# Optimization experiments

Hardware: AMD Instinct MI355X
Metric: run time of the kernel (lower is better)

Reference implementation:

```python
import jax, jax.numpy as jnp
import numpy as np

B, T, I, H, C = 512, 256, 128, 64, 3  # batch, seq_len, input_size, hidden_size, num_classes


def _lstm_dir(x, w_ih, w_hh, b, reverse):
    """Single-direction LSTM over x: (B, T, D_in) -> (B, T, H).

    Gate order matches PyTorch: i, f, g, o. b = b_ih + b_hh (combined).
    Input-to-gate GEMM is hoisted out of the scan for efficiency.
    """
    xg = jnp.einsum('bti,gi->btg', x, w_ih) + b  # (B, T, 4H)
    if reverse:
        xg = xg[:, ::-1]
    xg_t = jnp.swapaxes(xg, 0, 1)  # (T, B, 4H)
    h0 = jnp.zeros((x.shape[0], w_hh.shape[1]), x.dtype)
    c0 = jnp.zeros_like(h0)

    def step(carry, g):
        h, c = carry
        g = g + h @ w_hh.T
        i, f, gg, o = jnp.split(g, 4, axis=-1)
        i = jax.nn.sigmoid(i)
        f = jax.nn.sigmoid(f)
        gg = jnp.tanh(gg)
        o = jax.nn.sigmoid(o)
        c = f * c + i * gg
        h = o * jnp.tanh(c)
        return (h, c), h

    _, hs = jax.lax.scan(step, (h0, c0), xg_t)  # (T, B, H)
    hs = jnp.swapaxes(hs, 0, 1)  # (B, T, H)
    if reverse:
        hs = hs[:, ::-1]
    return hs


def setup_inputs() -> dict:
    key = jax.random.key(0)
    ks = jax.random.split(key, 20)
    s = 1.0 / np.sqrt(H)  # PyTorch LSTM init scale
    d = {"x": jax.random.normal(ks[0], (B, T, I), dtype=jnp.float32)}
    i = 1
    for l, d_in in [(0, I), (1, 2 * H)]:
        for suf in ["f", "r"]:
            d[f"w_ih_l{l}{suf}"] = jax.random.uniform(ks[i], (4 * H, d_in), minval=-s, maxval=s); i += 1
            d[f"w_hh_l{l}{suf}"] = jax.random.uniform(ks[i], (4 * H, H), minval=-s, maxval=s); i += 1
            d[f"b_l{l}{suf}"] = jax.random.uniform(ks[i], (4 * H,), minval=-s, maxval=s); i += 1
    d["fc_w"] = jax.random.uniform(ks[i], (C, 2 * H), minval=-s, maxval=s); i += 1
    d["fc_b"] = jax.random.uniform(ks[i], (C,), minval=-s, maxval=s)
    return d


def reference(x, w_ih_l0f, w_hh_l0f, b_l0f, w_ih_l0r, w_hh_l0r, b_l0r,
              w_ih_l1f, w_hh_l1f, b_l1f, w_ih_l1r, w_hh_l1r, b_l1r,
              fc_w, fc_b):
    # Layer 0 (bidirectional)
    h0f = _lstm_dir(x, w_ih_l0f, w_hh_l0f, b_l0f, False)
    h0r = _lstm_dir(x, w_ih_l0r, w_hh_l0r, b_l0r, True)
    x1 = jnp.concatenate([h0f, h0r], axis=-1)  # (B, T, 2H)
    # (inter-layer dropout is identity in eval mode)
    # Layer 1 (bidirectional)
    h1f = _lstm_dir(x1, w_ih_l1f, w_hh_l1f, b_l1f, False)
    h1r = _lstm_dir(x1, w_ih_l1r, w_hh_l1r, b_l1r, True)
    out = jnp.concatenate([h1f, h1r], axis=-1)  # (B, T, 2H)
    last = out[:, -1, :]  # (B, 2H); dropout is identity in eval mode
    return last @ fc_w.T + fc_b  # (B, C) logits
```

## Files before the change

### kernel.cpp

```cpp
#include <hip/hip_runtime.h>

#define TT 256
#define BB 512
#define NG 256
#define KIN 128

typedef _Float16 half2v __attribute__((ext_vector_type(2)));
typedef _Float16 half4v __attribute__((ext_vector_type(4)));
typedef _Float16 half8v __attribute__((ext_vector_type(8)));
typedef float float4v __attribute__((ext_vector_type(4)));

__device__ __forceinline__ float sig_(float x){ return 1.f/(1.f+__expf(-x)); }
__device__ __forceinline__ float th_(float x){ return fmaf(2.f, 1.f/(1.f+__expf(-2.f*x)), -1.f); }

#if __has_builtin(__builtin_amdgcn_fdot2)
__device__ __forceinline__ float fdot2_(half2v a, half2v b, float c){
  return __builtin_amdgcn_fdot2(a, b, c, false);
}
#else
__device__ __forceinline__ float fdot2_(half2v a, half2v b, float c){
  return c + (float)a[0]*(float)b[0] + (float)a[1]*(float)b[1];
}
#endif

#define SV2(v,k) __builtin_shufflevector((v),(v), 2*(k), 2*(k)+1)

__device__ __forceinline__ half4v ld4h(const float* p){
  float4v v = *reinterpret_cast<const float4v*>(p);
  half4v h; h[0]=(_Float16)v[0]; h[1]=(_Float16)v[1]; h[2]=(_Float16)v[2]; h[3]=(_Float16)v[3];
  return h;
}

__global__ __launch_bounds__(256)
void conv_weights(const float* __restrict__ s0, const float* __restrict__ s1,
                  const float* __restrict__ s2, const float* __restrict__ s3,
                  const float* __restrict__ s4, const float* __restrict__ s5,
                  _Float16* __restrict__ dst)
{
  const int bid = blockIdx.x, tid = threadIdx.x;
  const float* src; int off, idx;
  if (bid < 128)      { src=s0; off=0;      idx=bid*256+tid; }
  else if (bid < 256) { src=s1; off=32768;  idx=(bid-128)*256+tid; }
  else if (bid < 384) { src=s2; off=65536;  idx=(bid-256)*256+tid; }
  else if (bid < 448) { src=s3; off=98304;  idx=(bid-384)*256+tid; }
  else if (bid < 512) { src=s4; off=114688; idx=(bid-448)*256+tid; }
  else                { src=s5; off=131072; idx=(bid-512)*256+tid; }
  dst[off+idx] = (_Float16)src[idx];
}

template<typename AT>
__global__ __launch_bounds__(256)
void gemm_xg(const AT* __restrict__ A, const _Float16* __restrict__ W16,
             const float* __restrict__ bias, _Float16* __restrict__ Cout)
{
  __shared__ __align__(16) _Float16 aL[64][72];
  __shared__ __align__(16) _Float16 wL[256][72];
  const int tid  = threadIdx.x;
  const int wave = tid >> 6;
  const int lane = tid & 63;
  const int lr   = lane & 15;
  const int kg   = lane >> 4;
  const size_t m0 = (size_t)blockIdx.x * 64;

  float4v acc[4][4];
  #pragma unroll
  for (int a=0;a<4;a++)
    #pragma unroll
    for (int b=0;b<4;b++)
      acc[a][b] = float4v{0.f,0.f,0.f,0.f};

  for (int kc = 0; kc < KIN; kc += 64) {
    if constexpr (__is_same(AT, float)) {
      #pragma unroll
      for (int q=0;q<4;q++){
        int fi = tid + q*256;
        int r = fi >> 4, c4 = (fi & 15)*4;
        *reinterpret_cast<half4v*>(&aL[r][c4]) = ld4h(&A[(m0+(size_t)r)*KIN + kc + c4]);
      }
    } else {
      #pragma unroll
      for (int q=0;q<2;q++){
        int fi = tid + q*256;
        int r = fi >> 3, c8 = (fi & 7)*8;
        *reinterpret_cast<half8v*>(&aL[r][c8]) =
            *reinterpret_cast<const half8v*>(&A[(m0+(size_t)r)*KIN + kc + c8]);
      }
    }
    #pragma unroll
    for (int q=0;q<8;q++){
      int fi = tid + q*256;
      int n = fi >> 3, c8 = (fi & 7)*8;
      *reinterpret_cast<half8v*>(&wL[n][c8]) =
          *reinterpret_cast<const half8v*>(&W16[(size_t)n*KIN + kc + c8]);
    }
    __syncthreads();
    #pragma unroll
    for (int ks=0; ks<64; ks+=32){
      half8v af[4], bf[4];
      #pragma unroll
      for (int rt=0;rt<4;rt++)
        af[rt] = *reinterpret_cast<const half8v*>(&aL[rt*16+lr][ks + kg*8]);
      #pragma unroll
      for (int ct=0;ct<4;ct++)
        bf[ct] = *reinterpret_cast<const half8v*>(&wL[wave*64 + ct*16 + lr][ks + kg*8]);
      #pragma unroll
      for (int rt=0;rt<4;rt++)
        #pragma unroll
        for (int ct=0;ct<4;ct++)
          acc[rt][ct] = __builtin_amdgcn_mfma_f32_16x16x32_f16(af[rt], bf[ct], acc[rt][ct], 0,0,0);
    }
    __syncthreads();
  }
  #pragma unroll
  for (int ct=0;ct<4;ct++){
    const int col = wave*64 + ct*16 + lr;
    const float bv = bias[col];
    #pragma unroll
    for (int rt=0;rt<4;rt++){
      const size_t rbase = m0 + rt*16 + kg*4;
      #pragma unroll
      for (int i=0;i<4;i++)
        Cout[(rbase+(size_t)i)*NG + col] = (_Float16)(acc[rt][ct][i] + bv);
    }
  }
}

template<int MODE>
__global__ __launch_bounds__(64, 1)
void lstm_scan_w1(const _Float16* __restrict__ xgPool,
                  const _Float16* __restrict__ whhPool,
                  int nF,
                  _Float16* __restrict__ x1out, float* __restrict__ hfin)
{
  const int j = threadIdx.x;
  const bool rev = (int)blockIdx.x >= nF;
  const int b = rev ? ((int)blockIdx.x - nF) : (int)blockIdx.x;
  const size_t xgOff  = rev ? (size_t)BB*TT*NG : 0;
  const size_t whhOff = rev ? (size_t)16384 : 0;
  const _Float16* xg  = xgPool  + xgOff;
  const _Float16* whh = whhPool + whhOff;

  __shared__ __align__(16) _Float16 hs[64];

  half8v wi8[8], wf8[8], wg8[8], wo8[8];
  #pragma unroll
  for (int q=0;q<8;q++){
    wi8[q] = *reinterpret_cast<const half8v*>(&whh[(size_t)(      j)*64 + q*8]);
    wf8[q] = *reinterpret_cast<const half8v*>(&whh[(size_t)( 64 + j)*64 + q*8]);
    wg8[q] = *reinterpret_cast<const half8v*>(&whh[(size_t)(128 + j)*64 + q*8]);
    wo8[q] = *reinterpret_cast<const half8v*>(&whh[(size_t)(192 + j)*64 + q*8]);
  }
  hs[j] = (_Float16)0.f;
  float c = 0.f, h_last = 0.f;
  __syncthreads();

  const _Float16* xgb = xg + (size_t)b*TT*NG + j;
  _Float16 ring[4][4];
  #pragma unroll
  for (int u=0;u<4;u++){
    const size_t o = (size_t)(rev ? (TT-1-u) : u) * NG;
    #pragma unroll
    for (int g=0;g<4;g++) ring[u][g] = xgb[o + g*64];
  }

  for (int tb=0; tb<TT; tb+=4){
    #pragma unroll
    for (int u=0;u<4;u++){
      const int tt = tb + u;
      const int t  = rev ? (TT-1-tt) : tt;

      const float x0  = (float)ring[u][0];
      const float x1v = (float)ring[u][1];
      const float x2  = (float)ring[u][2];
      const float x3  = (float)ring[u][3];

      const int tf = tt + 4;
      if (tf < TT){
        const size_t o = (size_t)(rev ? (TT-1-tf) : tf) * NG;
        #pragma unroll
        for (int g=0;g<4;g++) ring[u][g] = xgb[o + g*64];
      }

      float ai=0.f, a2i=0.f, af=0.f, a2f=0.f, ag=0.f, a2g=0.f, ao=0.f, a2o=0.f;
      #pragma unroll
      for (int q=0;q<8;q++){
        const half8v h8 = *reinterpret_cast<const half8v*>(&hs[q*8]);
        const half2v hA = SV2(h8,0), hB = SV2(h8,1), hC = SV2(h8,2), hD = SV2(h8,3);
        ai  = fdot2_(SV2(wi8[q],0), hA, ai);  a2i = fdot2_(SV2(wi8[q],1), hB, a2i);
        ai  = fdot2_(SV2(wi8[q],2), hC, ai);  a2i = fdot2_(SV2(wi8[q],3), hD, a2i);
        af  = fdot2_(SV2(wf8[q],0), hA, af);  a2f = fdot2_(SV2(wf8[q],1), hB, a2f);
        af  = fdot2_(SV2(wf8[q],2), hC, af);  a2f = fdot2_(SV2(wf8[q],3), hD, a2f);
        ag  = fdot2_(SV2(wg8[q],0), hA, ag);  a2g = fdot2_(SV2(wg8[q],1), hB, a2g);
        ag  = fdot2_(SV2(wg8[q],2), hC, ag);  a2g = fdot2_(SV2(wg8[q],3), hD, a2g);
        ao  = fdot2_(SV2(wo8[q],0), hA, ao);  a2o = fdot2_(SV2(wo8[q],1), hB, a2o);
        ao  = fdot2_(SV2(wo8[q],2), hC, ao);  a2o = fdot2_(SV2(wo8[q],3), hD, a2o);
      }
      const float iv = sig_(x0  + (ai + a2i));
      const float fv = sig_(x1v + (af + a2f));
      const float gv = th_ (x2  + (ag + a2g));
      const float ov = sig_(x3  + (ao + a2o));

      c = fv*c + iv*gv;
      const float h = ov * th_(c);
      h_last = h;
      hs[j] = (_Float16)h;
      if constexpr (MODE==0)
        x1out[((size_t)b*TT + t)*128 + (rev ? 64 : 0) + j] = (_Float16)h;
    }
  }
  if constexpr (MODE==1)
    hfin[(size_t)b*64 + j] = h_last;
}

__global__ __launch_bounds__(256)
void final_fuse(const _Float16* __restrict__ x1, const float* __restrict__ w_ih,
                const float* __restrict__ bvec, const float* __restrict__ hfin,
                const float* __restrict__ fcw, const float* __restrict__ fcb,
                float* __restrict__ out)
{
  const int b = blockIdx.x, tid = threadIdx.x;
  __shared__ float xs[128];
  __shared__ float act[256];
  __shared__ float hall[128];
  if (tid < 128) xs[tid] = (float)x1[((size_t)b*TT + (TT-1))*128 + tid];
  __syncthreads();
  float a = bvec[tid];
  #pragma unroll
  for (int kk=0;kk<32;kk++){
    float4v wv = *reinterpret_cast<const float4v*>(&w_ih[(size_t)tid*128 + kk*4]);
    a += wv[0]*xs[kk*4] + wv[1]*xs[kk*4+1] + wv[2]*xs[kk*4+2] + wv[3]*xs[kk*4+3];
  }
  const int grp = tid>>6;
  act[tid] = (grp==2) ? th_(a) : sig_(a);
  __syncthreads();
  if (tid < 64) {
    float c = act[tid]*act[128+tid];
    float h = act[192+tid]*th_(c);
    hall[64+tid] = h;
    hall[tid] = hfin[(size_t)b*64 + tid];
  }
  __syncthreads();
  if (tid < 3) {
    float acc2 = fcb[tid];
    for (int k=0;k<128;k++) acc2 += fcw[(size_t)tid*128 + k]*hall[k];
    out[(size_t)b*3 + tid] = acc2;
  }
}

extern "C" void kernel_launch(void* const* d_in, const int* in_sizes, int n_in,
                              void* d_out, int out_size, void* d_ws, size_t ws_size,
                              hipStream_t stream) {
  const float* x        = (const float*)d_in[0];
  const float* w_ih_l0f = (const float*)d_in[1];
  const float* w_hh_l0f = (const float*)d_in[2];
  const float* b_l0f    = (const float*)d_in[3];
  const float* w_ih_l0r = (const float*)d_in[4];
  const float* w_hh_l0r = (const float*)d_in[5];
  const float* b_l0r    = (const float*)d_in[6];
  const float* w_ih_l1f = (const float*)d_in[7];
  const float* w_hh_l1f = (const float*)d_in[8];
  const float* b_l1f    = (const float*)d_in[9];
  const float* w_ih_l1r = (const float*)d_in[10];
  const float* b_l1r    = (const float*)d_in[12];
  const float* fc_w     = (const float*)d_in[13];
  const float* fc_b     = (const float*)d_in[14];
  float* out = (float*)d_out;

  const size_t XG_BYTES = (size_t)BB*TT*NG*2;
  const size_t X1_BYTES = (size_t)BB*TT*128*2;
  const size_t HF_BYTES = (size_t)BB*64*4;
  const size_t W16_BYTES = (size_t)147456*2;
  if (ws_size < 2*XG_BYTES + X1_BYTES + HF_BYTES + W16_BYTES) return;
  _Float16* xgF  = (_Float16*)d_ws;
  _Float16* xgR  = (_Float16*)((char*)d_ws + XG_BYTES);
  _Float16* x1   = (_Float16*)((char*)d_ws + 2*XG_BYTES);
  float*    hfin = (float*)   ((char*)d_ws + 2*XG_BYTES + X1_BYTES);
  _Float16* w16  = (_Float16*)((char*)d_ws + 2*XG_BYTES + X1_BYTES + HF_BYTES);
  _Float16* wih_l0f16 = w16;
  _Float16* wih_l0r16 = w16 + 32768;
  _Float16* wih_l1f16 = w16 + 65536;
  _Float16* whh_l0f16 = w16 + 98304;
  _Float16* whh_l1f16 = w16 + 131072;

  const int MBLK = (BB*TT)/64;

  conv_weights<<<576, 256, 0, stream>>>(w_ih_l0f, w_ih_l0r, w_ih_l1f,
                                        w_hh_l0f, w_hh_l0r, w_hh_l1f, w16);
  gemm_xg<float><<<MBLK, 256, 0, stream>>>(x, wih_l0f16, b_l0f, xgF);
  gemm_xg<float><<<MBLK, 256, 0, stream>>>(x, wih_l0r16, b_l0r, xgR);
  lstm_scan_w1<0><<<1024, 64, 0, stream>>>(xgF, whh_l0f16, 512, x1, nullptr);
  gemm_xg<_Float16><<<MBLK, 256, 0, stream>>>(x1, wih_l1f16, b_l1f, xgF);
  lstm_scan_w1<1><<<512, 64, 0, stream>>>(xgF, whh_l1f16, 512, nullptr, hfin);
  final_fuse<<<BB, 256, 0, stream>>>(x1, w_ih_l1r, b_l1r, hfin, fc_w, fc_b, out);
}
```

Measured before the change: 477.3 us.

## Split LSTM scan gates across four waves with LDS exchange per timestep

The recurrent scan now uses four waves per sequence instead of one. Each wave computes the h·W_hh dot product and activation for a single gate, writes it to a double-buffered LDS array, and after a block barrier every wave redundantly updates c and h. This cuts the serial dot-product work per thread per step by four and raises the number of resident waves per CU. The cost is a __syncthreads on every timestep, redundant cell-state math in all four waves, and a deeper xg prefetch ring.

```diff
diff --git a/kernel.cpp b/kernel.cpp
--- a/kernel.cpp
+++ b/kernel.cpp
@@ -126,90 +126,77 @@
 }
 
 template<int MODE>
-__global__ __launch_bounds__(64, 1)
-void lstm_scan_w1(const _Float16* __restrict__ xgPool,
+__global__ __launch_bounds__(256, 4)
+void lstm_scan_g4(const _Float16* __restrict__ xgPool,
                   const _Float16* __restrict__ whhPool,
                   int nF,
                   _Float16* __restrict__ x1out, float* __restrict__ hfin)
 {
-  const int j = threadIdx.x;
+  const int tid = threadIdx.x;
+  const int w   = tid >> 6;
+  const int j   = tid & 63;
   const bool rev = (int)blockIdx.x >= nF;
   const int b = rev ? ((int)blockIdx.x - nF) : (int)blockIdx.x;
-  const size_t xgOff  = rev ? (size_t)BB*TT*NG : 0;
-  const size_t whhOff = rev ? (size_t)16384 : 0;
-  const _Float16* xg  = xgPool  + xgOff;
-  const _Float16* whh = whhPool + whhOff;
-
-  __shared__ __align__(16) _Float16 hs[64];
-
-  half8v wi8[8], wf8[8], wg8[8], wo8[8];
-  #pragma unroll
-  for (int q=0;q<8;q++){
-    wi8[q] = *reinterpret_cast<const half8v*>(&whh[(size_t)(      j)*64 + q*8]);
-    wf8[q] = *reinterpret_cast<const half8v*>(&whh[(size_t)( 64 + j)*64 + q*8]);
-    wg8[q] = *reinterpret_cast<const half8v*>(&whh[(size_t)(128 + j)*64 + q*8]);
-    wo8[q] = *reinterpret_cast<const half8v*>(&whh[(size_t)(192 + j)*64 + q*8]);
-  }
-  hs[j] = (_Float16)0.f;
+  const _Float16* xg  = xgPool  + (rev ? (size_t)BB*TT*NG : 0);
+  const _Float16* whh = whhPool + (rev ? (size_t)16384 : 0);
+
+  __shared__ __align__(16) float acts[2][256];
+  __shared__ __align__(16) _Float16 hs4[4][64];
+
+  half8v wreg[8];
+  #pragma unroll
+  for (int q=0;q<8;q++)
+    wreg[q] = *reinterpret_cast<const half8v*>(&whh[(size_t)(w*64 + j)*64 + q*8]);
+
+  hs4[w][j] = (_Float16)0.f;
   float c = 0.f, h_last = 0.f;
-  __syncthreads();
-
-  const _Float16* xgb = xg + (size_t)b*TT*NG + j;
-  _Float16 ring[4][4];
-  #pragma unroll
-  for (int u=0;u<4;u++){
-    const size_t o = (size_t)(rev ? (TT-1-u) : u) * NG;
-    #pragma unroll
-    for (int g=0;g<4;g++) ring[u][g] = xgb[o + g*64];
-  }
-
-  for (int tb=0; tb<TT; tb+=4){
-    #pragma unroll
-    for (int u=0;u<4;u++){
+
+  const _Float16* xgb = xg + (size_t)b*TT*NG + w*64 + j;
+  _Float16 ring[8];
+  #pragma unroll
+  for (int u=0;u<8;u++)
+    ring[u] = xgb[(size_t)(rev ? (TT-1-u) : u) * NG];
+
+  for (int tb=0; tb<TT; tb+=8){
+    #pragma unroll
+    for (int u=0;u<8;u++){
       const int tt = tb + u;
       const int t  = rev ? (TT-1-tt) : tt;
 
-      const float x0  = (float)ring[u][0];
-      const float x1v = (float)ring[u][1];
-      const float x2  = (float)ring[u][2];
-      const float x3  = (float)ring[u][3];
-
-      const int tf = tt + 4;
-      if (tf < TT){
-        const size_t o = (size_t)(rev ? (TT-1-tf) : tf) * NG;
-        #pragma unroll
-        for (int g=0;g<4;g++) ring[u][g] = xgb[o + g*64];
+      const float xp = (float)ring[u];
+      const int tf = tt + 8;
+      if (tf < TT)
+        ring[u] = xgb[(size_t)(rev ? (TT-1-tf) : tf) * NG];
+
+      float a=0.f, a2=0.f;
+      #pragma unroll
+      for (int q=0;q<8;q++){
+        const half8v h8 = *reinterpret_cast<const half8v*>(&hs4[w][q*8]);
+        a  = fdot2_(SV2(wreg[q],0), SV2(h8,0), a);
+        a2 = fdot2_(SV2(wreg[q],1), SV2(h8,1), a2);
+        a  = fdot2_(SV2(wreg[q],2), SV2(h8,2), a);
+        a2 = fdot2_(SV2(wreg[q],3), SV2(h8,3), a2);
       }
-
-      float ai=0.f, a2i=0.f, af=0.f, a2f=0.f, ag=0.f, a2g=0.f, ao=0.f, a2o=0.f;
-      #pragma unroll
-      for (int q=0;q<8;q++){
-        const half8v h8 = *reinterpret_cast<const half8v*>(&hs[q*8]);
-        const half2v hA = SV2(h8,0), hB = SV2(h8,1), hC = SV2(h8,2), hD = SV2(h8,3);
-        ai  = fdot2_(SV2(wi8[q],0), hA, ai);  a2i = fdot2_(SV2(wi8[q],1), hB, a2i);
-        ai  = fdot2_(SV2(wi8[q],2), hC, ai);  a2i = fdot2_(SV2(wi8[q],3), hD, a2i);
-        af  = fdot2_(SV2(wf8[q],0), hA, af);  a2f = fdot2_(SV2(wf8[q],1), hB, a2f);
-        af  = fdot2_(SV2(wf8[q],2), hC, af);  a2f = fdot2_(SV2(wf8[q],3), hD, a2f);
-        ag  = fdot2_(SV2(wg8[q],0), hA, ag);  a2g = fdot2_(SV2(wg8[q],1), hB, a2g);
-        ag  = fdot2_(SV2(wg8[q],2), hC, ag);  a2g = fdot2_(SV2(wg8[q],3), hD, a2g);
-        ao  = fdot2_(SV2(wo8[q],0), hA, ao);  a2o = fdot2_(SV2(wo8[q],1), hB, a2o);
-        ao  = fdot2_(SV2(wo8[q],2), hC, ao);  a2o = fdot2_(SV2(wo8[q],3), hD, a2o);
-      }
-      const float iv = sig_(x0  + (ai + a2i));
-      const float fv = sig_(x1v + (af + a2f));
-      const float gv = th_ (x2  + (ag + a2g));
-      const float ov = sig_(x3  + (ao + a2o));
-
+      const float pre = xp + (a + a2);
+      acts[tt&1][w*64 + j] = (w==2) ? th_(pre) : sig_(pre);
+      __syncthreads();
+
+      const float iv = acts[tt&1][j];
+      const float fv = acts[tt&1][64+j];
+      const float gv = acts[tt&1][128+j];
+      const float ov = acts[tt&1][192+j];
       c = fv*c + iv*gv;
       const float h = ov * th_(c);
       h_last = h;
-      hs[j] = (_Float16)h;
+      hs4[w][j] = (_Float16)h;
       if constexpr (MODE==0)
-        x1out[((size_t)b*TT + t)*128 + (rev ? 64 : 0) + j] = (_Float16)h;
+        if (w == 0)
+          x1out[((size_t)b*TT + t)*128 + (rev ? 64 : 0) + j] = (_Float16)h;
     }
   }
   if constexpr (MODE==1)
-    hfin[(size_t)b*64 + j] = h_last;
+    if (w == 0)
+      hfin[(size_t)b*64 + j] = h_last;
 }
 
 __global__ __launch_bounds__(256)
@@ -288,8 +275,8 @@
                                         w_hh_l0f, w_hh_l0r, w_hh_l1f, w16);
   gemm_xg<float><<<MBLK, 256, 0, stream>>>(x, wih_l0f16, b_l0f, xgF);
   gemm_xg<float><<<MBLK, 256, 0, stream>>>(x, wih_l0r16, b_l0r, xgR);
-  lstm_scan_w1<0><<<1024, 64, 0, stream>>>(xgF, whh_l0f16, 512, x1, nullptr);
+  lstm_scan_g4<0><<<1024, 256, 0, stream>>>(xgF, whh_l0f16, 512, x1, nullptr);
   gemm_xg<_Float16><<<MBLK, 256, 0, stream>>>(x1, wih_l1f16, b_l1f, xgF);
-  lstm_scan_w1<1><<<512, 64, 0, stream>>>(xgF, whh_l1f16, 512, nullptr, hfin);
+  lstm_scan_g4<1><<<512, 256, 0, stream>>>(xgF, whh_l1f16, 512, nullptr, hfin);
   final_fuse<<<BB, 256, 0, stream>>>(x1, w_ih_l1r, b_l1r, hfin, fc_w, fc_b, out);
 }
```

Measured after the change: 402.8 us. -15.6%, faster.
